# Kernel optimization log

Measured on AMD Instinct MI355X. Metric: run time of the kernel, lower is better.

The kernel has to match this reference:

```python
import jax, jax.numpy as jnp
import numpy as np

N = 200000
F = 64   # input_node_features_size
H = 64   # input_node_hidden_state_size
E = 64   # input_edge_hidden_state_size
DEG = 16
OUT = 128          # output_node_hidden_state_size
HALF = OUT // 2    # 64
IN1 = F + H        # 128 (first_layer=False -> concat)
MID1 = (F + H + HALF) // 2  # 96


def setup_inputs() -> dict:
    key = jax.random.key(0)
    ks = jax.random.split(key, 11)
    s = lambda fan_in: 1.0 / np.sqrt(fan_in)
    return {
        "node_features": jax.random.normal(ks[0], (N, F), jnp.float32),
        "node_hidden": jax.random.normal(ks[1], (N, H), jnp.float32),
        "mailbox": jax.random.normal(ks[2], (N, DEG, E), jnp.float32),
        # net_1: Linear(IN1->MID1), Linear(MID1->HALF)
        "w1a": jax.random.uniform(ks[3], (IN1, MID1), jnp.float32, -s(IN1), s(IN1)),
        "b1a": jax.random.uniform(ks[4], (MID1,), jnp.float32, -s(IN1), s(IN1)),
        "w1b": jax.random.uniform(ks[5], (MID1, HALF), jnp.float32, -s(MID1), s(MID1)),
        "b1b": jax.random.uniform(ks[6], (HALF,), jnp.float32, -s(MID1), s(MID1)),
        # net_2: Linear(E->HALF), Linear(HALF->HALF)
        "w2a": jax.random.uniform(ks[7], (E, HALF), jnp.float32, -s(E), s(E)),
        "b2a": jax.random.uniform(ks[8], (HALF,), jnp.float32, -s(E), s(E)),
        "w2b": jax.random.uniform(ks[9], (HALF, HALF), jnp.float32, -s(HALF), s(HALF)),
        "b2b": jax.random.uniform(ks[10], (HALF,), jnp.float32, -s(HALF), s(HALF)),
    }


def reference(node_features, node_hidden, mailbox,
              w1a, b1a, w1b, b1b, w2a, b2a, w2b, b2b):
    # Branch 1: concat(features, hidden) -> Linear -> ReLU -> Linear -> Tanh
    # (dropout is identity at inference)
    x1 = jnp.concatenate([node_features, node_hidden], axis=1)  # [N, IN1]
    h1 = jax.nn.relu(x1 @ w1a + b1a)                            # [N, MID1]
    r1 = jnp.tanh(h1 @ w1b + b1b)                               # [N, HALF]

    # Branch 2: mailbox sum-aggregate -> Linear -> ReLU -> Linear -> Tanh
    x2 = jnp.sum(mailbox, axis=1)                               # [N, E]
    h2 = jax.nn.relu(x2 @ w2a + b2a)                            # [N, HALF]
    r2 = jnp.tanh(h2 @ w2b + b2b)                               # [N, HALF]

    # Concat + per-row L2 (Frobenius over dim=1) normalize
    r = jnp.concatenate([r1, r2], axis=1)                       # [N, OUT]
    norm = jnp.linalg.norm(r, axis=1, keepdims=True)
    return r / norm
```

## Files before the change

### kernel.cpp

```cpp
#include <hip/hip_runtime.h>

constexpr int NB = 64;
constexpr int THREADS = 256;
constexpr int X1SU = 66;
constexpr int H1SU = 50;
constexpr int X2S  = 68;

typedef __fp16 half2_t __attribute__((ext_vector_type(2)));

__device__ __forceinline__ float fast_tanh(float x) {
    float e = __expf(2.0f * x);
    return 1.0f - 2.0f * __builtin_amdgcn_rcpf(e + 1.0f);
}

__device__ __forceinline__ unsigned pk16(float a, float b) {
    half2_t h = __builtin_amdgcn_cvt_pkrtz(a, b);
    return __builtin_bit_cast(unsigned, h);
}

__device__ __forceinline__ void fma24(float x0, float x1, float x2, float x3,
                                      const float* __restrict__ w0,
                                      float* __restrict__ acc) {
    #pragma unroll
    for (int j = 0; j < 24; ++j) acc[j] = fmaf(x0, w0[j],       acc[j]);
    #pragma unroll
    for (int j = 0; j < 24; ++j) acc[j] = fmaf(x1, w0[96 + j],  acc[j]);
    #pragma unroll
    for (int j = 0; j < 24; ++j) acc[j] = fmaf(x2, w0[192 + j], acc[j]);
    #pragma unroll
    for (int j = 0; j < 24; ++j) acc[j] = fmaf(x3, w0[288 + j], acc[j]);
}

__device__ __forceinline__ void fma16(float x0, float x1, float x2, float x3,
                                      const float* __restrict__ w0,
                                      float* __restrict__ acc) {
    #pragma unroll
    for (int j = 0; j < 16; ++j) acc[j] = fmaf(x0, w0[j],       acc[j]);
    #pragma unroll
    for (int j = 0; j < 16; ++j) acc[j] = fmaf(x1, w0[64 + j],  acc[j]);
    #pragma unroll
    for (int j = 0; j < 16; ++j) acc[j] = fmaf(x2, w0[128 + j], acc[j]);
    #pragma unroll
    for (int j = 0; j < 16; ++j) acc[j] = fmaf(x3, w0[192 + j], acc[j]);
}

__global__ __launch_bounds__(THREADS) void node_net_kernel(
    const float* __restrict__ feat, const float* __restrict__ hid,
    const float* __restrict__ mail,
    const float* __restrict__ w1a, const float* __restrict__ b1a,
    const float* __restrict__ w1b, const float* __restrict__ b1b,
    const float* __restrict__ w2a, const float* __restrict__ b2a,
    const float* __restrict__ w2b, const float* __restrict__ b2b,
    float* __restrict__ out)
{
    __shared__ unsigned ldsA[NB * X1SU];
    __shared__ float    ldsB[NB * X2S];
    __shared__ float    ldsS[NB * 4];

    const int t  = threadIdx.x;
    const int n0 = blockIdx.x * NB;
    const int c4 = t & 15;
    const int nb = t >> 4;

    const float4* mb0 = reinterpret_cast<const float4*>(mail) + (size_t)(n0 + nb) * 256 + c4;

    #pragma unroll
    for (int i = 0; i < 4; ++i) {
        int n = nb + 16 * i;
        float4 f = reinterpret_cast<const float4*>(feat)[(size_t)(n0 + n) * 16 + c4];
        float4 g = reinterpret_cast<const float4*>(hid )[(size_t)(n0 + n) * 16 + c4];
        unsigned* dst = &ldsA[n * X1SU];
        *reinterpret_cast<uint2*>(dst + c4 * 2)      = make_uint2(pk16(f.x, f.y), pk16(f.z, f.w));
        *reinterpret_cast<uint2*>(dst + 32 + c4 * 2) = make_uint2(pk16(g.x, g.y), pk16(g.z, g.w));
    }
    __syncthreads();

    const int node = t & 63;
    const int sub  = __builtin_amdgcn_readfirstlane(t >> 6);

    float acc1[24];
    {
        const float* b = b1a + sub * 24;
        #pragma unroll
        for (int j = 0; j < 24; ++j) acc1[j] = b[j];
    }
    {
        const unsigned* xr = &ldsA[node * X1SU];
        #pragma unroll 1
        for (int c = 0; c < 4; ++c) {
            const float4* chain = mb0 + (size_t)c * 4096;
            float4 m;
            #pragma unroll
            for (int half = 0; half < 2; ++half) {
                float4 cur[8];
                #pragma unroll
                for (int d = 0; d < 8; ++d)
                    cur[d] = chain[(half * 8 + d) * 16];
                __builtin_amdgcn_sched_barrier(0);
                #pragma unroll
                for (int kk = 0; kk < 4; ++kk) {
                    int k4 = (c * 2 + half) * 4 + kk;
                    uint2 xu = *reinterpret_cast<const uint2*>(xr + 2 * k4);
                    half2_t p0 = __builtin_bit_cast(half2_t, xu.x);
                    half2_t p1 = __builtin_bit_cast(half2_t, xu.y);
                    fma24((float)p0.x, (float)p0.y, (float)p1.x, (float)p1.y,
                          w1a + (k4 * 4) * 96 + sub * 24, acc1);
                }
                __builtin_amdgcn_sched_barrier(0);
                float4 s = ((cur[0] + cur[1]) + (cur[2] + cur[3]))
                         + ((cur[4] + cur[5]) + (cur[6] + cur[7]));
                if (half == 0) m = s; else m += s;
            }
            *reinterpret_cast<float4*>(&ldsB[(nb + 16 * c) * X2S + c4 * 4]) = m;
        }
    }
    __syncthreads();
    {
        unsigned* hv = &ldsA[node * H1SU + sub * 12];
        #pragma unroll
        for (int p = 0; p < 12; ++p)
            hv[p] = pk16(fmaxf(acc1[2*p], 0.f), fmaxf(acc1[2*p + 1], 0.f));
    }
    __syncthreads();

    float r1v[16];
    {
        float acc[16];
        const float* b = b1b + sub * 16;
        #pragma unroll
        for (int j = 0; j < 16; ++j) acc[j] = b[j];
        const unsigned* hb = &ldsA[node * H1SU];
        #pragma unroll 2
        for (int k4 = 0; k4 < 24; ++k4) {
            uint2 hu = *reinterpret_cast<const uint2*>(hb + 2 * k4);
            half2_t p0 = __builtin_bit_cast(half2_t, hu.x);
            half2_t p1 = __builtin_bit_cast(half2_t, hu.y);
            fma16((float)p0.x, (float)p0.y, (float)p1.x, (float)p1.y,
                  w1b + (k4 * 4) * 64 + sub * 16, acc);
        }
        #pragma unroll
        for (int j = 0; j < 16; ++j) r1v[j] = fast_tanh(acc[j]);
    }

    float h2v[16];
    {
        float acc[16];
        const float* b = b2a + sub * 16;
        #pragma unroll
        for (int j = 0; j < 16; ++j) acc[j] = b[j];
        const float4* xr = reinterpret_cast<const float4*>(&ldsB[node * X2S]);
        #pragma unroll 2
        for (int k4 = 0; k4 < 16; ++k4) {
            float4 x = xr[k4];
            fma16(x.x, x.y, x.z, x.w, w2a + (k4 * 4) * 64 + sub * 16, acc);
        }
        #pragma unroll
        for (int j = 0; j < 16; ++j) h2v[j] = fmaxf(acc[j], 0.f);
    }
    __syncthreads();
    {
        float4* hrow = reinterpret_cast<float4*>(&ldsB[node * X2S + sub * 16]);
        hrow[0] = make_float4(h2v[0],  h2v[1],  h2v[2],  h2v[3]);
        hrow[1] = make_float4(h2v[4],  h2v[5],  h2v[6],  h2v[7]);
        hrow[2] = make_float4(h2v[8],  h2v[9],  h2v[10], h2v[11]);
        hrow[3] = make_float4(h2v[12], h2v[13], h2v[14], h2v[15]);
    }
    __syncthreads();

    float r2v[16];
    {
        float acc[16];
        const float* b = b2b + sub * 16;
        #pragma unroll
        for (int j = 0; j < 16; ++j) acc[j] = b[j];
        const float4* hr = reinterpret_cast<const float4*>(&ldsB[node * X2S]);
        #pragma unroll 2
        for (int k4 = 0; k4 < 16; ++k4) {
            float4 x = hr[k4];
            fma16(x.x, x.y, x.z, x.w, w2b + (k4 * 4) * 64 + sub * 16, acc);
        }
        #pragma unroll
        for (int j = 0; j < 16; ++j) r2v[j] = fast_tanh(acc[j]);
    }

    float s = 0.f;
    #pragma unroll
    for (int j = 0; j < 16; ++j) s = fmaf(r1v[j], r1v[j], s);
    #pragma unroll
    for (int j = 0; j < 16; ++j) s = fmaf(r2v[j], r2v[j], s);
    ldsS[node * 4 + sub] = s;
    __syncthreads();
    float4 sv = reinterpret_cast<const float4*>(ldsS)[node];
    float rn = rsqrtf(sv.x + sv.y + sv.z + sv.w);

    float* orow = out + (size_t)(n0 + node) * 128;
    float4* o1 = reinterpret_cast<float4*>(orow + sub * 16);
    float4* o2 = reinterpret_cast<float4*>(orow + 64 + sub * 16);
    #pragma unroll
    for (int j4 = 0; j4 < 4; ++j4) {
        o1[j4] = make_float4(r1v[j4*4+0]*rn, r1v[j4*4+1]*rn, r1v[j4*4+2]*rn, r1v[j4*4+3]*rn);
        o2[j4] = make_float4(r2v[j4*4+0]*rn, r2v[j4*4+1]*rn, r2v[j4*4+2]*rn, r2v[j4*4+3]*rn);
    }
}

extern "C" void kernel_launch(void* const* d_in, const int* in_sizes, int n_in,
                              void* d_out, int out_size, void* d_ws, size_t ws_size,
                              hipStream_t stream) {
    const float* feat = (const float*)d_in[0];
    const float* hid  = (const float*)d_in[1];
    const float* mail = (const float*)d_in[2];
    const float* w1a  = (const float*)d_in[3];
    const float* b1a  = (const float*)d_in[4];
    const float* w1b  = (const float*)d_in[5];
    const float* b1b  = (const float*)d_in[6];
    const float* w2a  = (const float*)d_in[7];
    const float* b2a  = (const float*)d_in[8];
    const float* w2b  = (const float*)d_in[9];
    const float* b2b  = (const float*)d_in[10];
    float* out = (float*)d_out;

    const int N = in_sizes[0] / 64;
    const int blocks = N / NB;

    node_net_kernel<<<blocks, THREADS, 0, stream>>>(
        feat, hid, mail, w1a, b1a, w1b, b1b, w2a, b2a, w2b, b2b, out);
}
```

Before: 239.9 us.

## Spread mailbox loads across layer-1 and layer-1b matmul phases

The mailbox streaming is rebalanced so that only 12 of the 16 neighbour rows are loaded during the first-layer matmul. The last 4 rows per chain are loaded and accumulated during the second matmul (w1b), read-modify-writing the partial sums in LDS. This is meant to overlap more global memory latency with compute across both phases and reduce register pressure in the first loop. It adds an extra LDS read-modify-write and a barrier before the branch-2 matmul.

Result: slower. 249.1 us (+3.8%).

```diff
diff --git a/kernel.cpp b/kernel.cpp
--- a/kernel.cpp
+++ b/kernel.cpp
@@ -89,28 +89,39 @@
         #pragma unroll 1
         for (int c = 0; c < 4; ++c) {
             const float4* chain = mb0 + (size_t)c * 4096;
-            float4 m;
-            #pragma unroll
-            for (int half = 0; half < 2; ++half) {
-                float4 cur[8];
-                #pragma unroll
-                for (int d = 0; d < 8; ++d)
-                    cur[d] = chain[(half * 8 + d) * 16];
-                __builtin_amdgcn_sched_barrier(0);
-                #pragma unroll
-                for (int kk = 0; kk < 4; ++kk) {
-                    int k4 = (c * 2 + half) * 4 + kk;
-                    uint2 xu = *reinterpret_cast<const uint2*>(xr + 2 * k4);
-                    half2_t p0 = __builtin_bit_cast(half2_t, xu.x);
-                    half2_t p1 = __builtin_bit_cast(half2_t, xu.y);
-                    fma24((float)p0.x, (float)p0.y, (float)p1.x, (float)p1.y,
-                          w1a + (k4 * 4) * 96 + sub * 24, acc1);
-                }
-                __builtin_amdgcn_sched_barrier(0);
-                float4 s = ((cur[0] + cur[1]) + (cur[2] + cur[3]))
-                         + ((cur[4] + cur[5]) + (cur[6] + cur[7]));
-                if (half == 0) m = s; else m += s;
+            float4 curA[8];
+            #pragma unroll
+            for (int d = 0; d < 8; ++d)
+                curA[d] = chain[d * 16];
+            __builtin_amdgcn_sched_barrier(0);
+            #pragma unroll
+            for (int kk = 0; kk < 4; ++kk) {
+                int k4 = c * 8 + kk;
+                uint2 xu = *reinterpret_cast<const uint2*>(xr + 2 * k4);
+                half2_t p0 = __builtin_bit_cast(half2_t, xu.x);
+                half2_t p1 = __builtin_bit_cast(half2_t, xu.y);
+                fma24((float)p0.x, (float)p0.y, (float)p1.x, (float)p1.y,
+                      w1a + (k4 * 4) * 96 + sub * 24, acc1);
             }
+            __builtin_amdgcn_sched_barrier(0);
+            float4 m = ((curA[0] + curA[1]) + (curA[2] + curA[3]))
+                     + ((curA[4] + curA[5]) + (curA[6] + curA[7]));
+            float4 curB[4];
+            #pragma unroll
+            for (int d = 0; d < 4; ++d)
+                curB[d] = chain[(8 + d) * 16];
+            __builtin_amdgcn_sched_barrier(0);
+            #pragma unroll
+            for (int kk = 4; kk < 8; ++kk) {
+                int k4 = c * 8 + kk;
+                uint2 xu = *reinterpret_cast<const uint2*>(xr + 2 * k4);
+                half2_t p0 = __builtin_bit_cast(half2_t, xu.x);
+                half2_t p1 = __builtin_bit_cast(half2_t, xu.y);
+                fma24((float)p0.x, (float)p0.y, (float)p1.x, (float)p1.y,
+                      w1a + (k4 * 4) * 96 + sub * 24, acc1);
+            }
+            __builtin_amdgcn_sched_barrier(0);
+            m += (curB[0] + curB[1]) + (curB[2] + curB[3]);
             *reinterpret_cast<float4*>(&ldsB[(nb + 16 * c) * X2S + c4 * 4]) = m;
         }
     }
@@ -130,17 +141,33 @@
         #pragma unroll
         for (int j = 0; j < 16; ++j) acc[j] = b[j];
         const unsigned* hb = &ldsA[node * H1SU];
-        #pragma unroll 2
-        for (int k4 = 0; k4 < 24; ++k4) {
-            uint2 hu = *reinterpret_cast<const uint2*>(hb + 2 * k4);
-            half2_t p0 = __builtin_bit_cast(half2_t, hu.x);
-            half2_t p1 = __builtin_bit_cast(half2_t, hu.y);
-            fma16((float)p0.x, (float)p0.y, (float)p1.x, (float)p1.y,
-                  w1b + (k4 * 4) * 64 + sub * 16, acc);
+        #pragma unroll 1
+        for (int c = 0; c < 4; ++c) {
+            const float4* chain = mb0 + (size_t)c * 4096;
+            float4 cur[4];
+            #pragma unroll
+            for (int d = 0; d < 4; ++d)
+                cur[d] = chain[(12 + d) * 16];
+            __builtin_amdgcn_sched_barrier(0);
+            #pragma unroll
+            for (int kk = 0; kk < 6; ++kk) {
+                int k4 = c * 6 + kk;
+                uint2 hu = *reinterpret_cast<const uint2*>(hb + 2 * k4);
+                half2_t p0 = __builtin_bit_cast(half2_t, hu.x);
+                half2_t p1 = __builtin_bit_cast(half2_t, hu.y);
+                fma16((float)p0.x, (float)p0.y, (float)p1.x, (float)p1.y,
+                      w1b + (k4 * 4) * 64 + sub * 16, acc);
+            }
+            __builtin_amdgcn_sched_barrier(0);
+            float4* row = reinterpret_cast<float4*>(&ldsB[(nb + 16 * c) * X2S + c4 * 4]);
+            float4 m = *row;
+            m += (cur[0] + cur[1]) + (cur[2] + cur[3]);
+            *row = m;
         }
         #pragma unroll
         for (int j = 0; j < 16; ++j) r1v[j] = fast_tanh(acc[j]);
     }
+    __syncthreads();
 
     float h2v[16];
     {
```

## Make kernel persistent and prefetch next tile's mailbox during current tile compute

Applied to the files above, without the earlier changes.

Converts the kernel to a persistent grid of 1024 blocks that loop over node tiles with stride 1024. Each iteration spreads the mailbox loads and sum for the next tile across the layer-1a, 1b and 2a FMA loops, then stages the result in LDS for the next iteration. The goal is to hide the dominant mailbox HBM traffic behind compute and cut block launch overhead. The cost is extra register pressure, added barriers, and a fixed grid size that may not suit every CU count.

Result: slower. 867.9 us (+261.7%).

```diff
diff --git a/kernel.cpp b/kernel.cpp
--- a/kernel.cpp
+++ b/kernel.cpp
@@ -51,55 +51,90 @@
     const float* __restrict__ w1b, const float* __restrict__ b1b,
     const float* __restrict__ w2a, const float* __restrict__ b2a,
     const float* __restrict__ w2b, const float* __restrict__ b2b,
-    float* __restrict__ out)
+    float* __restrict__ out, int n_tiles)
 {
     __shared__ unsigned ldsA[NB * X1SU];
     __shared__ float    ldsB[NB * X2S];
     __shared__ float    ldsS[NB * 4];
 
-    const int t  = threadIdx.x;
-    const int n0 = blockIdx.x * NB;
-    const int c4 = t & 15;
-    const int nb = t >> 4;
-
-    const float4* mb0 = reinterpret_cast<const float4*>(mail) + (size_t)(n0 + nb) * 256 + c4;
-
-    #pragma unroll
-    for (int i = 0; i < 4; ++i) {
-        int n = nb + 16 * i;
-        float4 f = reinterpret_cast<const float4*>(feat)[(size_t)(n0 + n) * 16 + c4];
-        float4 g = reinterpret_cast<const float4*>(hid )[(size_t)(n0 + n) * 16 + c4];
-        unsigned* dst = &ldsA[n * X1SU];
-        *reinterpret_cast<uint2*>(dst + c4 * 2)      = make_uint2(pk16(f.x, f.y), pk16(f.z, f.w));
-        *reinterpret_cast<uint2*>(dst + 32 + c4 * 2) = make_uint2(pk16(g.x, g.y), pk16(g.z, g.w));
+    const int t    = threadIdx.x;
+    const int c4   = t & 15;
+    const int nb   = t >> 4;
+    const int node = t & 63;
+    const int sub  = __builtin_amdgcn_readfirstlane(t >> 6);
+    const int base = blockIdx.x;
+    const int nt   = (n_tiles - 1 - base) / 1024 + 1;
+
+    const float4* mail_f4 = reinterpret_cast<const float4*>(mail);
+
+    float4 macc[4];
+
+    {
+        const float4* mb = mail_f4 + ((size_t)base * NB + nb) * 256 + c4;
+        #pragma unroll
+        for (int i = 0; i < 4; ++i) macc[i] = make_float4(0.f, 0.f, 0.f, 0.f);
+        #pragma unroll 1
+        for (int j = 0; j < 8; ++j) {
+            float4 cur[8];
+            #pragma unroll
+            for (int c = 0; c < 4; ++c) {
+                const float4* ch = mb + (size_t)c * 4096 + (size_t)(2 * j) * 16;
+                cur[c]     = ch[0];
+                cur[4 + c] = ch[16];
+            }
+            #pragma unroll
+            for (int i = 0; i < 4; ++i) macc[i] += cur[i] + cur[4 + i];
+        }
+        #pragma unroll
+        for (int i = 0; i < 4; ++i)
+            *reinterpret_cast<float4*>(&ldsB[(nb + 16 * i) * X2S + c4 * 4]) = macc[i];
     }
     __syncthreads();
 
-    const int node = t & 63;
-    const int sub  = __builtin_amdgcn_readfirstlane(t >> 6);
-
-    float acc1[24];
-    {
-        const float* b = b1a + sub * 24;
-        #pragma unroll
-        for (int j = 0; j < 24; ++j) acc1[j] = b[j];
-    }
-    {
-        const unsigned* xr = &ldsA[node * X1SU];
-        #pragma unroll 1
-        for (int c = 0; c < 4; ++c) {
-            const float4* chain = mb0 + (size_t)c * 4096;
-            float4 m;
-            #pragma unroll
-            for (int half = 0; half < 2; ++half) {
+    #pragma unroll 1
+    for (int k = 0; k < nt; ++k) {
+        const size_t n0 = (size_t)(base + 1024 * k) * NB;
+        const bool hn = (k + 1 < nt);
+        const float4* mbN = hn
+            ? mail_f4 + ((size_t)(base + 1024 * (k + 1)) * NB + nb) * 256 + c4
+            : mail_f4 + nb * 256 + c4;
+
+        #pragma unroll
+        for (int i = 0; i < 4; ++i) {
+            int n = nb + 16 * i;
+            float4 f = reinterpret_cast<const float4*>(feat)[(n0 + n) * 16 + c4];
+            float4 g = reinterpret_cast<const float4*>(hid )[(n0 + n) * 16 + c4];
+            unsigned* dst = &ldsA[n * X1SU];
+            *reinterpret_cast<uint2*>(dst + c4 * 2)      = make_uint2(pk16(f.x, f.y), pk16(f.z, f.w));
+            *reinterpret_cast<uint2*>(dst + 32 + c4 * 2) = make_uint2(pk16(g.x, g.y), pk16(g.z, g.w));
+        }
+        __syncthreads();
+
+        float acc1[24];
+        {
+            const float* b = b1a + sub * 24;
+            #pragma unroll
+            for (int j = 0; j < 24; ++j) acc1[j] = b[j];
+        }
+        #pragma unroll
+        for (int i = 0; i < 4; ++i) macc[i] = make_float4(0.f, 0.f, 0.f, 0.f);
+        {
+            const unsigned* xr = &ldsA[node * X1SU];
+            #pragma unroll 1
+            for (int bj = 0; bj < 4; ++bj) {
                 float4 cur[8];
+                if (hn) {
+                    #pragma unroll
+                    for (int c = 0; c < 4; ++c) {
+                        const float4* ch = mbN + (size_t)c * 4096 + (size_t)(2 * bj) * 16;
+                        cur[c]     = ch[0];
+                        cur[4 + c] = ch[16];
+                    }
+                }
+                __builtin_amdgcn_sched_barrier(0);
                 #pragma unroll
-                for (int d = 0; d < 8; ++d)
-                    cur[d] = chain[(half * 8 + d) * 16];
-                __builtin_amdgcn_sched_barrier(0);
-                #pragma unroll
-                for (int kk = 0; kk < 4; ++kk) {
-                    int k4 = (c * 2 + half) * 4 + kk;
+                for (int kk = 0; kk < 8; ++kk) {
+                    int k4 = bj * 8 + kk;
                     uint2 xu = *reinterpret_cast<const uint2*>(xr + 2 * k4);
                     half2_t p0 = __builtin_bit_cast(half2_t, xu.x);
                     half2_t p1 = __builtin_bit_cast(half2_t, xu.y);
@@ -107,99 +142,143 @@
                           w1a + (k4 * 4) * 96 + sub * 24, acc1);
                 }
                 __builtin_amdgcn_sched_barrier(0);
-                float4 s = ((cur[0] + cur[1]) + (cur[2] + cur[3]))
-                         + ((cur[4] + cur[5]) + (cur[6] + cur[7]));
-                if (half == 0) m = s; else m += s;
-            }
-            *reinterpret_cast<float4*>(&ldsB[(nb + 16 * c) * X2S + c4 * 4]) = m;
-        }
-    }
-    __syncthreads();
-    {
-        unsigned* hv = &ldsA[node * H1SU + sub * 12];
-        #pragma unroll
-        for (int p = 0; p < 12; ++p)
-            hv[p] = pk16(fmaxf(acc1[2*p], 0.f), fmaxf(acc1[2*p + 1], 0.f));
-    }
-    __syncthreads();
-
-    float r1v[16];
-    {
-        float acc[16];
-        const float* b = b1b + sub * 16;
-        #pragma unroll
-        for (int j = 0; j < 16; ++j) acc[j] = b[j];
-        const unsigned* hb = &ldsA[node * H1SU];
-        #pragma unroll 2
-        for (int k4 = 0; k4 < 24; ++k4) {
-            uint2 hu = *reinterpret_cast<const uint2*>(hb + 2 * k4);
-            half2_t p0 = __builtin_bit_cast(half2_t, hu.x);
-            half2_t p1 = __builtin_bit_cast(half2_t, hu.y);
-            fma16((float)p0.x, (float)p0.y, (float)p1.x, (float)p1.y,
-                  w1b + (k4 * 4) * 64 + sub * 16, acc);
-        }
-        #pragma unroll
-        for (int j = 0; j < 16; ++j) r1v[j] = fast_tanh(acc[j]);
-    }
-
-    float h2v[16];
-    {
-        float acc[16];
-        const float* b = b2a + sub * 16;
-        #pragma unroll
-        for (int j = 0; j < 16; ++j) acc[j] = b[j];
-        const float4* xr = reinterpret_cast<const float4*>(&ldsB[node * X2S]);
-        #pragma unroll 2
-        for (int k4 = 0; k4 < 16; ++k4) {
-            float4 x = xr[k4];
-            fma16(x.x, x.y, x.z, x.w, w2a + (k4 * 4) * 64 + sub * 16, acc);
-        }
-        #pragma unroll
-        for (int j = 0; j < 16; ++j) h2v[j] = fmaxf(acc[j], 0.f);
-    }
-    __syncthreads();
-    {
-        float4* hrow = reinterpret_cast<float4*>(&ldsB[node * X2S + sub * 16]);
-        hrow[0] = make_float4(h2v[0],  h2v[1],  h2v[2],  h2v[3]);
-        hrow[1] = make_float4(h2v[4],  h2v[5],  h2v[6],  h2v[7]);
-        hrow[2] = make_float4(h2v[8],  h2v[9],  h2v[10], h2v[11]);
-        hrow[3] = make_float4(h2v[12], h2v[13], h2v[14], h2v[15]);
-    }
-    __syncthreads();
-
-    float r2v[16];
-    {
-        float acc[16];
-        const float* b = b2b + sub * 16;
-        #pragma unroll
-        for (int j = 0; j < 16; ++j) acc[j] = b[j];
-        const float4* hr = reinterpret_cast<const float4*>(&ldsB[node * X2S]);
-        #pragma unroll 2
-        for (int k4 = 0; k4 < 16; ++k4) {
-            float4 x = hr[k4];
-            fma16(x.x, x.y, x.z, x.w, w2b + (k4 * 4) * 64 + sub * 16, acc);
-        }
-        #pragma unroll
-        for (int j = 0; j < 16; ++j) r2v[j] = fast_tanh(acc[j]);
-    }
-
-    float s = 0.f;
-    #pragma unroll
-    for (int j = 0; j < 16; ++j) s = fmaf(r1v[j], r1v[j], s);
-    #pragma unroll
-    for (int j = 0; j < 16; ++j) s = fmaf(r2v[j], r2v[j], s);
-    ldsS[node * 4 + sub] = s;
-    __syncthreads();
-    float4 sv = reinterpret_cast<const float4*>(ldsS)[node];
-    float rn = rsqrtf(sv.x + sv.y + sv.z + sv.w);
-
-    float* orow = out + (size_t)(n0 + node) * 128;
-    float4* o1 = reinterpret_cast<float4*>(orow + sub * 16);
-    float4* o2 = reinterpret_cast<float4*>(orow + 64 + sub * 16);
-    #pragma unroll
-    for (int j4 = 0; j4 < 4; ++j4) {
-        o1[j4] = make_float4(r1v[j4*4+0]*rn, r1v[j4*4+1]*rn, r1v[j4*4+2]*rn, r1v[j4*4+3]*rn);
-        o2[j4] = make_float4(r2v[j4*4+0]*rn, r2v[j4*4+1]*rn, r2v[j4*4+2]*rn, r2v[j4*4+3]*rn);
+                if (hn) {
+                    #pragma unroll
+                    for (int i = 0; i < 4; ++i) macc[i] += cur[i] + cur[4 + i];
+                }
+            }
+        }
+        __syncthreads();
+        {
+            unsigned* hv = &ldsA[node * H1SU + sub * 12];
+            #pragma unroll
+            for (int p = 0; p < 12; ++p)
+                hv[p] = pk16(fmaxf(acc1[2*p], 0.f), fmaxf(acc1[2*p + 1], 0.f));
+        }
+        __syncthreads();
+
+        float r1v[16];
+        {
+            float acc[16];
+            const float* b = b1b + sub * 16;
+            #pragma unroll
+            for (int j = 0; j < 16; ++j) acc[j] = b[j];
+            const unsigned* hb = &ldsA[node * H1SU];
+            #pragma unroll 1
+            for (int bj = 0; bj < 2; ++bj) {
+                float4 cur[8];
+                if (hn) {
+                    #pragma unroll
+                    for (int c = 0; c < 4; ++c) {
+                        const float4* ch = mbN + (size_t)c * 4096 + (size_t)(8 + 2 * bj) * 16;
+                        cur[c]     = ch[0];
+                        cur[4 + c] = ch[16];
+                    }
+                }
+                __builtin_amdgcn_sched_barrier(0);
+                #pragma unroll
+                for (int kk = 0; kk < 12; ++kk) {
+                    int k4 = bj * 12 + kk;
+                    uint2 hu = *reinterpret_cast<const uint2*>(hb + 2 * k4);
+                    half2_t p0 = __builtin_bit_cast(half2_t, hu.x);
+                    half2_t p1 = __builtin_bit_cast(half2_t, hu.y);
+                    fma16((float)p0.x, (float)p0.y, (float)p1.x, (float)p1.y,
+                          w1b + (k4 * 4) * 64 + sub * 16, acc);
+                }
+                __builtin_amdgcn_sched_barrier(0);
+                if (hn) {
+                    #pragma unroll
+                    for (int i = 0; i < 4; ++i) macc[i] += cur[i] + cur[4 + i];
+                }
+            }
+            #pragma unroll
+            for (int j = 0; j < 16; ++j) r1v[j] = fast_tanh(acc[j]);
+        }
+
+        float h2v[16];
+        {
+            float acc[16];
+            const float* b = b2a + sub * 16;
+            #pragma unroll
+            for (int j = 0; j < 16; ++j) acc[j] = b[j];
+            const float4* xr = reinterpret_cast<const float4*>(&ldsB[node * X2S]);
+            #pragma unroll 1
+            for (int bj = 0; bj < 2; ++bj) {
+                float4 cur[8];
+                if (hn) {
+                    #pragma unroll
+                    for (int c = 0; c < 4; ++c) {
+                        const float4* ch = mbN + (size_t)c * 4096 + (size_t)(12 + 2 * bj) * 16;
+                        cur[c]     = ch[0];
+                        cur[4 + c] = ch[16];
+                    }
+                }
+                __builtin_amdgcn_sched_barrier(0);
+                #pragma unroll
+                for (int kk = 0; kk < 8; ++kk) {
+                    int k4 = bj * 8 + kk;
+                    float4 x = xr[k4];
+                    fma16(x.x, x.y, x.z, x.w, w2a + (k4 * 4) * 64 + sub * 16, acc);
+                }
+                __builtin_amdgcn_sched_barrier(0);
+                if (hn) {
+                    #pragma unroll
+                    for (int i = 0; i < 4; ++i) macc[i] += cur[i] + cur[4 + i];
+                }
+            }
+            #pragma unroll
+            for (int j = 0; j < 16; ++j) h2v[j] = fmaxf(acc[j], 0.f);
+        }
+        __syncthreads();
+        {
+            float4* hrow = reinterpret_cast<float4*>(&ldsB[node * X2S + sub * 16]);
+            hrow[0] = make_float4(h2v[0],  h2v[1],  h2v[2],  h2v[3]);
+            hrow[1] = make_float4(h2v[4],  h2v[5],  h2v[6],  h2v[7]);
+            hrow[2] = make_float4(h2v[8],  h2v[9],  h2v[10], h2v[11]);
+            hrow[3] = make_float4(h2v[12], h2v[13], h2v[14], h2v[15]);
+        }
+        __syncthreads();
+
+        float r2v[16];
+        {
+            float acc[16];
+            const float* b = b2b + sub * 16;
+            #pragma unroll
+            for (int j = 0; j < 16; ++j) acc[j] = b[j];
+            const float4* hr = reinterpret_cast<const float4*>(&ldsB[node * X2S]);
+            #pragma unroll 2
+            for (int k4 = 0; k4 < 16; ++k4) {
+                float4 x = hr[k4];
+                fma16(x.x, x.y, x.z, x.w, w2b + (k4 * 4) * 64 + sub * 16, acc);
+            }
+            #pragma unroll
+            for (int j = 0; j < 16; ++j) r2v[j] = fast_tanh(acc[j]);
+        }
+        __syncthreads();
+
+        float s = 0.f;
+        #pragma unroll
+        for (int j = 0; j < 16; ++j) s = fmaf(r1v[j], r1v[j], s);
+        #pragma unroll
+        for (int j = 0; j < 16; ++j) s = fmaf(r2v[j], r2v[j], s);
+        ldsS[node * 4 + sub] = s;
+        if (hn) {
+            #pragma unroll
+            for (int i = 0; i < 4; ++i)
+                *reinterpret_cast<float4*>(&ldsB[(nb + 16 * i) * X2S + c4 * 4]) = macc[i];
+        }
+        __syncthreads();
+        float4 sv = reinterpret_cast<const float4*>(ldsS)[node];
+        float rn = rsqrtf(sv.x + sv.y + sv.z + sv.w);
+
+        float* orow = out + (n0 + node) * 128;
+        float4* o1 = reinterpret_cast<float4*>(orow + sub * 16);
+        float4* o2 = reinterpret_cast<float4*>(orow + 64 + sub * 16);
+        #pragma unroll
+        for (int j4 = 0; j4 < 4; ++j4) {
+            o1[j4] = make_float4(r1v[j4*4+0]*rn, r1v[j4*4+1]*rn, r1v[j4*4+2]*rn, r1v[j4*4+3]*rn);
+            o2[j4] = make_float4(r2v[j4*4+0]*rn, r2v[j4*4+1]*rn, r2v[j4*4+2]*rn, r2v[j4*4+3]*rn);
+        }
     }
 }
 
@@ -220,8 +299,9 @@
     float* out = (float*)d_out;
 
     const int N = in_sizes[0] / 64;
-    const int blocks = N / NB;
+    const int n_tiles = N / NB;
+    const int blocks = 1024;
 
     node_net_kernel<<<blocks, THREADS, 0, stream>>>(
-        feat, hid, mail, w1a, b1a, w1b, b1b, w2a, b2a, w2b, b2b, out);
-}
+        feat, hid, mail, w1a, b1a, w1b, b1b, w2a, b2a, w2b, b2b, out, n_tiles);
+}
```

## Pack weights to fp16 pairs and use fdot2 for all four matmuls

Applied to the files above, without the earlier changes.

Adds a small pre-kernel that converts the four weight matrices into packed fp16 pairs, stored in the workspace and interleaved along the K dimension. The main kernel then replaces scalar fp32 FMAs with v_dot2 fp16 instructions, halving both the instruction count and the weight bytes loaded. The mailbox sum and the branch-2 hidden activations are also stored in LDS as fp16, which shrinks LDS use. The cost is an extra kernel launch per call and reduced precision for the weights and branch-2 inputs.

Measured after the change: 232.0 us. 3.3% less time.

```diff
diff --git a/kernel.cpp b/kernel.cpp
--- a/kernel.cpp
+++ b/kernel.cpp
@@ -4,7 +4,13 @@
 constexpr int THREADS = 256;
 constexpr int X1SU = 66;
 constexpr int H1SU = 50;
-constexpr int X2S  = 68;
+constexpr int X2SU = 35;
+
+constexpr int W1A_OFF = 0;
+constexpr int W1B_OFF = 6144;
+constexpr int W2A_OFF = 9216;
+constexpr int W2B_OFF = 11264;
+constexpr int WTOTAL  = 13312;
 
 typedef __fp16 half2_t __attribute__((ext_vector_type(2)));
 
@@ -18,43 +24,55 @@
     return __builtin_bit_cast(unsigned, h);
 }
 
-__device__ __forceinline__ void fma24(float x0, float x1, float x2, float x3,
-                                      const float* __restrict__ w0,
+__device__ __forceinline__ half2_t uh(unsigned u) {
+    return __builtin_bit_cast(half2_t, u);
+}
+
+__device__ __forceinline__ void dot24(half2_t pa, half2_t pb,
+                                      const unsigned* __restrict__ w0,
+                                      const unsigned* __restrict__ w1,
                                       float* __restrict__ acc) {
     #pragma unroll
-    for (int j = 0; j < 24; ++j) acc[j] = fmaf(x0, w0[j],       acc[j]);
-    #pragma unroll
-    for (int j = 0; j < 24; ++j) acc[j] = fmaf(x1, w0[96 + j],  acc[j]);
-    #pragma unroll
-    for (int j = 0; j < 24; ++j) acc[j] = fmaf(x2, w0[192 + j], acc[j]);
-    #pragma unroll
-    for (int j = 0; j < 24; ++j) acc[j] = fmaf(x3, w0[288 + j], acc[j]);
-}
-
-__device__ __forceinline__ void fma16(float x0, float x1, float x2, float x3,
-                                      const float* __restrict__ w0,
+    for (int j = 0; j < 24; ++j) acc[j] = __builtin_amdgcn_fdot2(pa, uh(w0[j]), acc[j], false);
+    #pragma unroll
+    for (int j = 0; j < 24; ++j) acc[j] = __builtin_amdgcn_fdot2(pb, uh(w1[j]), acc[j], false);
+}
+
+__device__ __forceinline__ void dot16(half2_t pa, half2_t pb,
+                                      const unsigned* __restrict__ w0,
+                                      const unsigned* __restrict__ w1,
                                       float* __restrict__ acc) {
     #pragma unroll
-    for (int j = 0; j < 16; ++j) acc[j] = fmaf(x0, w0[j],       acc[j]);
-    #pragma unroll
-    for (int j = 0; j < 16; ++j) acc[j] = fmaf(x1, w0[64 + j],  acc[j]);
-    #pragma unroll
-    for (int j = 0; j < 16; ++j) acc[j] = fmaf(x2, w0[128 + j], acc[j]);
-    #pragma unroll
-    for (int j = 0; j < 16; ++j) acc[j] = fmaf(x3, w0[192 + j], acc[j]);
+    for (int j = 0; j < 16; ++j) acc[j] = __builtin_amdgcn_fdot2(pa, uh(w0[j]), acc[j], false);
+    #pragma unroll
+    for (int j = 0; j < 16; ++j) acc[j] = __builtin_amdgcn_fdot2(pb, uh(w1[j]), acc[j], false);
+}
+
+__global__ __launch_bounds__(256) void cvt_weights(
+    const float* __restrict__ w1a, const float* __restrict__ w1b,
+    const float* __restrict__ w2a, const float* __restrict__ w2b,
+    unsigned* __restrict__ wp)
+{
+    int idx = blockIdx.x * 256 + threadIdx.x;
+    const float* src; int cols, rel;
+    if (idx < W1B_OFF)      { rel = idx;           src = w1a; cols = 96; }
+    else if (idx < W2A_OFF) { rel = idx - W1B_OFF; src = w1b; cols = 64; }
+    else if (idx < W2B_OFF) { rel = idx - W2A_OFF; src = w2a; cols = 64; }
+    else                    { rel = idx - W2B_OFF; src = w2b; cols = 64; }
+    int k2 = rel / cols, j = rel - k2 * cols;
+    wp[idx] = pk16(src[(2 * k2) * cols + j], src[(2 * k2 + 1) * cols + j]);
 }
 
 __global__ __launch_bounds__(THREADS) void node_net_kernel(
     const float* __restrict__ feat, const float* __restrict__ hid,
     const float* __restrict__ mail,
-    const float* __restrict__ w1a, const float* __restrict__ b1a,
-    const float* __restrict__ w1b, const float* __restrict__ b1b,
-    const float* __restrict__ w2a, const float* __restrict__ b2a,
-    const float* __restrict__ w2b, const float* __restrict__ b2b,
+    const float* __restrict__ b1a, const float* __restrict__ b1b,
+    const float* __restrict__ b2a, const float* __restrict__ b2b,
+    const unsigned* __restrict__ wp,
     float* __restrict__ out)
 {
     __shared__ unsigned ldsA[NB * X1SU];
-    __shared__ float    ldsB[NB * X2S];
+    __shared__ unsigned ldsB[NB * X2SU];
     __shared__ float    ldsS[NB * 4];
 
     const int t  = threadIdx.x;
@@ -86,6 +104,7 @@
     }
     {
         const unsigned* xr = &ldsA[node * X1SU];
+        const unsigned* w1aP = wp + W1A_OFF + sub * 24;
         #pragma unroll 1
         for (int c = 0; c < 4; ++c) {
             const float4* chain = mb0 + (size_t)c * 4096;
@@ -101,17 +120,16 @@
                 for (int kk = 0; kk < 4; ++kk) {
                     int k4 = (c * 2 + half) * 4 + kk;
                     uint2 xu = *reinterpret_cast<const uint2*>(xr + 2 * k4);
-                    half2_t p0 = __builtin_bit_cast(half2_t, xu.x);
-                    half2_t p1 = __builtin_bit_cast(half2_t, xu.y);
-                    fma24((float)p0.x, (float)p0.y, (float)p1.x, (float)p1.y,
-                          w1a + (k4 * 4) * 96 + sub * 24, acc1);
+                    dot24(uh(xu.x), uh(xu.y),
+                          w1aP + (2 * k4) * 96, w1aP + (2 * k4 + 1) * 96, acc1);
                 }
                 __builtin_amdgcn_sched_barrier(0);
                 float4 s = ((cur[0] + cur[1]) + (cur[2] + cur[3]))
                          + ((cur[4] + cur[5]) + (cur[6] + cur[7]));
                 if (half == 0) m = s; else m += s;
             }
-            *reinterpret_cast<float4*>(&ldsB[(nb + 16 * c) * X2S + c4 * 4]) = m;
+            *reinterpret_cast<uint2*>(&ldsB[(nb + 16 * c) * X2SU + c4 * 2]) =
+                make_uint2(pk16(m.x, m.y), pk16(m.z, m.w));
         }
     }
     __syncthreads();
@@ -130,13 +148,12 @@
         #pragma unroll
         for (int j = 0; j < 16; ++j) acc[j] = b[j];
         const unsigned* hb = &ldsA[node * H1SU];
+        const unsigned* w1bP = wp + W1B_OFF + sub * 16;
         #pragma unroll 2
         for (int k4 = 0; k4 < 24; ++k4) {
-            uint2 hu = *reinterpret_cast<const uint2*>(hb + 2 * k4);
-            half2_t p0 = __builtin_bit_cast(half2_t, hu.x);
-            half2_t p1 = __builtin_bit_cast(half2_t, hu.y);
-            fma16((float)p0.x, (float)p0.y, (float)p1.x, (float)p1.y,
-                  w1b + (k4 * 4) * 64 + sub * 16, acc);
+            uint2 hu2 = *reinterpret_cast<const uint2*>(hb + 2 * k4);
+            dot16(uh(hu2.x), uh(hu2.y),
+                  w1bP + (2 * k4) * 64, w1bP + (2 * k4 + 1) * 64, acc);
         }
         #pragma unroll
         for (int j = 0; j < 16; ++j) r1v[j] = fast_tanh(acc[j]);
@@ -148,22 +165,23 @@
         const float* b = b2a + sub * 16;
         #pragma unroll
         for (int j = 0; j < 16; ++j) acc[j] = b[j];
-        const float4* xr = reinterpret_cast<const float4*>(&ldsB[node * X2S]);
+        const unsigned* xb = &ldsB[node * X2SU];
+        const unsigned* w2aP = wp + W2A_OFF + sub * 16;
         #pragma unroll 2
         for (int k4 = 0; k4 < 16; ++k4) {
-            float4 x = xr[k4];
-            fma16(x.x, x.y, x.z, x.w, w2a + (k4 * 4) * 64 + sub * 16, acc);
+            uint2 xu = *reinterpret_cast<const uint2*>(xb + 2 * k4);
+            dot16(uh(xu.x), uh(xu.y),
+                  w2aP + (2 * k4) * 64, w2aP + (2 * k4 + 1) * 64, acc);
         }
         #pragma unroll
         for (int j = 0; j < 16; ++j) h2v[j] = fmaxf(acc[j], 0.f);
     }
     __syncthreads();
     {
-        float4* hrow = reinterpret_cast<float4*>(&ldsB[node * X2S + sub * 16]);
-        hrow[0] = make_float4(h2v[0],  h2v[1],  h2v[2],  h2v[3]);
-        hrow[1] = make_float4(h2v[4],  h2v[5],  h2v[6],  h2v[7]);
-        hrow[2] = make_float4(h2v[8],  h2v[9],  h2v[10], h2v[11]);
-        hrow[3] = make_float4(h2v[12], h2v[13], h2v[14], h2v[15]);
+        unsigned* hrow = &ldsB[node * X2SU + sub * 8];
+        #pragma unroll
+        for (int p = 0; p < 8; ++p)
+            hrow[p] = pk16(h2v[2*p], h2v[2*p + 1]);
     }
     __syncthreads();
 
@@ -173,11 +191,13 @@
         const float* b = b2b + sub * 16;
         #pragma unroll
         for (int j = 0; j < 16; ++j) acc[j] = b[j];
-        const float4* hr = reinterpret_cast<const float4*>(&ldsB[node * X2S]);
+        const unsigned* hb2 = &ldsB[node * X2SU];
+        const unsigned* w2bP = wp + W2B_OFF + sub * 16;
         #pragma unroll 2
         for (int k4 = 0; k4 < 16; ++k4) {
-            float4 x = hr[k4];
-            fma16(x.x, x.y, x.z, x.w, w2b + (k4 * 4) * 64 + sub * 16, acc);
+            uint2 xu = *reinterpret_cast<const uint2*>(hb2 + 2 * k4);
+            dot16(uh(xu.x), uh(xu.y),
+                  w2bP + (2 * k4) * 64, w2bP + (2 * k4 + 1) * 64, acc);
         }
         #pragma unroll
         for (int j = 0; j < 16; ++j) r2v[j] = fast_tanh(acc[j]);
@@ -218,10 +238,12 @@
     const float* w2b  = (const float*)d_in[9];
     const float* b2b  = (const float*)d_in[10];
     float* out = (float*)d_out;
+    unsigned* wp = (unsigned*)d_ws;
 
     const int N = in_sizes[0] / 64;
     const int blocks = N / NB;
 
+    cvt_weights<<<WTOTAL / 256, 256, 0, stream>>>(w1a, w1b, w2a, w2b, wp);
     node_net_kernel<<<blocks, THREADS, 0, stream>>>(
-        feat, hid, mail, w1a, b1a, w1b, b1b, w2a, b2a, w2b, b2b, out);
-}
+        feat, hid, mail, b1a, b1b, b2a, b2b, wp, out);
+}
```
